# Performance work log

Measured on AMD Instinct MI355X. Metric: run time of the kernel, lower is better.

The kernel has to match this reference:

```python
import jax, jax.numpy as jnp
import numpy as np

N_NODES = 50000
N_EDGES = 800000
EDGE_F = 96
NODE_F = 256
GLOB_F = 64
HIDDEN = 1024
N_GRAPHS = 8
MLP_IN = NODE_F + 3 * EDGE_F + GLOB_F  # 608


def setup_inputs() -> dict:
    key = jax.random.key(0)
    ks = jax.random.split(key, 9)
    x = jax.random.normal(ks[0], (N_NODES, NODE_F), dtype=jnp.float32)
    edge_attr = jax.random.normal(ks[1], (N_EDGES, EDGE_F), dtype=jnp.float32)
    u = jax.random.normal(ks[2], (N_GRAPHS, GLOB_F), dtype=jnp.float32)
    W1 = jax.random.normal(ks[3], (MLP_IN, HIDDEN), dtype=jnp.float32) * (1.0 / np.sqrt(MLP_IN))
    b1 = jax.random.normal(ks[4], (HIDDEN,), dtype=jnp.float32) * 0.01
    W2 = jax.random.normal(ks[5], (HIDDEN, NODE_F), dtype=jnp.float32) * (1.0 / np.sqrt(HIDDEN))
    b2 = jax.random.normal(ks[6], (NODE_F,), dtype=jnp.float32) * 0.01
    edge_index = jax.random.randint(ks[7], (2, N_EDGES), 0, N_NODES, dtype=jnp.int64 if jax.config.jax_enable_x64 else jnp.int32)
    batch = jnp.sort(jax.random.randint(ks[8], (N_NODES,), 0, N_GRAPHS, dtype=jnp.int32))
    return {"x": x, "edge_attr": edge_attr, "u": u, "W1": W1, "b1": b1,
            "W2": W2, "b2": b2, "edge_index": edge_index, "batch": batch}


def reference(x, edge_attr, u, W1, b1, W2, b2, edge_index, batch):
    col = edge_index[1]  # destination node for each edge
    n = x.shape[0]
    # sum / max / mean segment reductions over edges -> per-node features
    out1 = jax.ops.segment_sum(edge_attr, col, num_segments=n)                     # [N, E_F]
    cnt = jax.ops.segment_sum(jnp.ones((edge_attr.shape[0], 1), edge_attr.dtype), col, num_segments=n)  # [N,1]
    out2 = jax.ops.segment_max(edge_attr, col, num_segments=n)
    out2 = jnp.where(cnt > 0, out2, jnp.zeros_like(out2))  # torch_scatter gives 0 for empty segments
    out3 = out1 / jnp.maximum(cnt, 1.0)                    # mean; 0 for empty segments
    h = jnp.concatenate([x, out1, out2, out3, u[batch]], axis=1)  # [N, 608]
    h = jax.nn.relu(h @ W1 + b1) @ W2 + b2                        # node MLP
    return h + x  # residual
```

## Files before the change

### kernel.cpp

```cpp
#include <hip/hip_runtime.h>
#include <stdint.h>

#define N_NODES 50000
#define N_EDGES 800000
#define EDGE_F  96
#define NODE_F  256
#define GLOB_F  64
#define HIDDEN  1024
#define MLP_IN  608
#define M_PAD   50048

typedef __bf16 bf16;
typedef __bf16 bf16x8 __attribute__((ext_vector_type(8)));
typedef float  f32x4  __attribute__((ext_vector_type(4)));

typedef __attribute__((address_space(1))) unsigned int gu32;
typedef __attribute__((address_space(3))) unsigned int lu32;

__device__ __forceinline__ void glds16(const void* g, void* l) {
    __builtin_amdgcn_global_load_lds((const gu32*)g, (lu32*)l, 16, 0, 0);
}

static constexpr size_t H_OFF    = 0;
static constexpr size_t H_BYTES  = (size_t)M_PAD * MLP_IN * 2;
static constexpr size_t HID_OFF  = H_OFF + H_BYTES;
static constexpr size_t HID_BYTES= (size_t)M_PAD * HIDDEN * 2;
static constexpr size_t W1T_OFF  = HID_OFF + HID_BYTES;
static constexpr size_t W1T_BYTES= (size_t)HIDDEN * MLP_IN * 2;
static constexpr size_t W2T_OFF  = W1T_OFF + W1T_BYTES;
static constexpr size_t W2T_BYTES= (size_t)NODE_F * HIDDEN * 2;
static constexpr size_t DEG_OFF  = W2T_OFF + W2T_BYTES;
static constexpr size_t DEG_BYTES= 200192;
static constexpr size_t CUR_OFF  = DEG_OFF + DEG_BYTES;
static constexpr size_t CUR_BYTES= 200192;
static constexpr size_t START_OFF= CUR_OFF + CUR_BYTES;
static constexpr size_t START_BYTES = 200192;
static constexpr size_t EIDS_OFF = START_OFF + START_BYTES;
static constexpr size_t EIDS_BYTES = (size_t)N_EDGES * 4;

__global__ __launch_bounds__(256) void hist_kernel(const int* __restrict__ col,
                                                   int* __restrict__ deg) {
    int e = blockIdx.x * 256 + threadIdx.x;
    if (e < N_EDGES) atomicAdd(&deg[col[e]], 1);
}

__global__ __launch_bounds__(1024) void scan_kernel(const int* __restrict__ deg,
                                                    int* __restrict__ start) {
    __shared__ int partial[1024];
    const int t = threadIdx.x;
    const int CH = 49;
    int base = t * CH;
    int s = 0;
    for (int i = 0; i < CH; i++) {
        int idx = base + i;
        if (idx < N_NODES) s += deg[idx];
    }
    partial[t] = s;
    __syncthreads();
    for (int off = 1; off < 1024; off <<= 1) {
        int v = (t >= off) ? partial[t - off] : 0;
        __syncthreads();
        partial[t] += v;
        __syncthreads();
    }
    int run = (t == 0) ? 0 : partial[t - 1];
    for (int i = 0; i < CH; i++) {
        int idx = base + i;
        if (idx < N_NODES) { start[idx] = run; run += deg[idx]; }
    }
    if (t == 1023) start[N_NODES] = run;
}

__global__ __launch_bounds__(256) void scatter_kernel(const int* __restrict__ col,
                                                      const int* __restrict__ start,
                                                      int* __restrict__ cursor,
                                                      int* __restrict__ eids) {
    int e = blockIdx.x * 256 + threadIdx.x;
    if (e < N_EDGES) {
        int c = col[e];
        int p = start[c] + atomicAdd(&cursor[c], 1);
        eids[p] = e;
    }
}

#define BH_CHUNK 128
__global__ __launch_bounds__(128) void build_h_kernel(const float* __restrict__ x,
                                                      const float* __restrict__ edge_attr,
                                                      const float* __restrict__ u,
                                                      const int* __restrict__ batch,
                                                      const int* __restrict__ start,
                                                      const int* __restrict__ eids,
                                                      bf16* __restrict__ H) {
    const int n = blockIdx.x;
    const int t = threadIdx.x;
    bf16* row = H + (size_t)n * MLP_IN;
    if (n >= N_NODES) {
        for (int c = t; c < MLP_IN; c += 128) row[c] = (bf16)0.0f;
        return;
    }
    if (t < 64) {
        float4 v = ((const float4*)(x + (size_t)n * NODE_F))[t];
        row[t * 4 + 0] = (bf16)v.x;
        row[t * 4 + 1] = (bf16)v.y;
        row[t * 4 + 2] = (bf16)v.z;
        row[t * 4 + 3] = (bf16)v.w;
    } else {
        int g = batch[n];
        row[544 + (t - 64)] = (bf16)u[g * GLOB_F + (t - 64)];
    }

    __shared__ int se[BH_CHUNK];
    const int s0 = start[n], s1 = start[n + 1];
    float sm = 0.0f, mx = -3.0e38f;
    for (int base = s0; base < s1; base += BH_CHUNK) {
        const int cnt = min(BH_CHUNK, s1 - base);
        __syncthreads();
        if (t < cnt) se[t] = eids[base + t];
        __syncthreads();
        if (t < EDGE_F) {
            int i = 0;
            for (; i + 4 <= cnt; i += 4) {
                float v0 = edge_attr[(size_t)se[i + 0] * EDGE_F + t];
                float v1 = edge_attr[(size_t)se[i + 1] * EDGE_F + t];
                float v2 = edge_attr[(size_t)se[i + 2] * EDGE_F + t];
                float v3 = edge_attr[(size_t)se[i + 3] * EDGE_F + t];
                sm += (v0 + v1) + (v2 + v3);
                mx = fmaxf(mx, fmaxf(fmaxf(v0, v1), fmaxf(v2, v3)));
            }
            for (; i < cnt; i++) {
                float v = edge_attr[(size_t)se[i] * EDGE_F + t];
                sm += v;
                mx = fmaxf(mx, v);
            }
        }
    }
    if (t < EDGE_F) {
        int d = s1 - s0;
        if (d == 0) mx = 0.0f;
        float mean = sm / fmaxf((float)d, 1.0f);
        row[256 + t] = (bf16)sm;
        row[352 + t] = (bf16)mx;
        row[448 + t] = (bf16)mean;
    }
}

__global__ __launch_bounds__(256) void convert_w_kernel(const float* __restrict__ W1,
                                                        const float* __restrict__ W2,
                                                        bf16* __restrict__ W1t,
                                                        bf16* __restrict__ W2t) {
    int i = blockIdx.x * 256 + threadIdx.x;
    if (i < HIDDEN * MLP_IN) {
        int n = i / MLP_IN, k = i - n * MLP_IN;
        W1t[i] = (bf16)W1[(size_t)k * HIDDEN + n];
    }
    if (i < NODE_F * HIDDEN) {
        int n = i / HIDDEN, k = i - n * HIDDEN;
        W2t[i] = (bf16)W2[(size_t)k * NODE_F + n];
    }
}

__global__ __launch_bounds__(256) void gemm1_kernel(const bf16* __restrict__ H,
                                                    const bf16* __restrict__ Wt,
                                                    const float* __restrict__ b1,
                                                    bf16* __restrict__ hid) {
    __shared__ __align__(16) bf16 As[128 * 32];
    __shared__ __align__(16) bf16 Bs[128 * 32];
    const int t = threadIdx.x;
    const int wave = t >> 6, lane = t & 63;
    const int quad = lane >> 4, l16 = lane & 15;
    const int wm = (wave & 1) << 6, wn = (wave >> 1) << 6;
    const int bm = blockIdx.x, bn = blockIdx.y;

    f32x4 acc[4][4] = {};

    const char* Ag = (const char*)H  + (size_t)bm * 128 * (MLP_IN * 2);
    const char* Bg = (const char*)Wt + (size_t)bn * 128 * (MLP_IN * 2);
    const int srow = t >> 2, scc = t & 3;
    const size_t rowoff = (size_t)srow * (MLP_IN * 2) + scc * 16;
    char* Al = (char*)As + t * 16;
    char* Bl = (char*)Bs + t * 16;

    for (int k0 = 0; k0 < MLP_IN; k0 += 32) {
        __syncthreads();
        const char* a0 = Ag + rowoff + k0 * 2;
        glds16(a0, Al);
        glds16(a0 + (size_t)64 * (MLP_IN * 2), Al + 4096);
        const char* b0 = Bg + rowoff + k0 * 2;
        glds16(b0, Bl);
        glds16(b0 + (size_t)64 * (MLP_IN * 2), Bl + 4096);
        __syncthreads();
        bf16x8 a[4], b[4];
#pragma unroll
        for (int i = 0; i < 4; i++) a[i] = *(const bf16x8*)&As[(wm + i * 16 + l16) * 32 + quad * 8];
#pragma unroll
        for (int i = 0; i < 4; i++) b[i] = *(const bf16x8*)&Bs[(wn + i * 16 + l16) * 32 + quad * 8];
#pragma unroll
        for (int i = 0; i < 4; i++)
#pragma unroll
            for (int j = 0; j < 4; j++)
                acc[i][j] = __builtin_amdgcn_mfma_f32_16x16x32_bf16(a[i], b[j], acc[i][j], 0, 0, 0);
    }
#pragma unroll
    for (int i = 0; i < 4; i++) {
        int row0 = bm * 128 + wm + i * 16 + quad * 4;
#pragma unroll
        for (int j = 0; j < 4; j++) {
            int col = bn * 128 + wn + j * 16 + l16;
            float bias = b1[col];
#pragma unroll
            for (int r = 0; r < 4; r++) {
                float v = acc[i][j][r] + bias;
                v = fmaxf(v, 0.0f);
                hid[(size_t)(row0 + r) * HIDDEN + col] = (bf16)v;
            }
        }
    }
}

__global__ __launch_bounds__(256) void gemm2_kernel(const bf16* __restrict__ Hd,
                                                    const bf16* __restrict__ Wt,
                                                    const float* __restrict__ b2,
                                                    const float* __restrict__ x,
                                                    float* __restrict__ out) {
    __shared__ __align__(16) bf16 As[128 * 32];
    __shared__ __align__(16) bf16 Bs[128 * 32];
    const int t = threadIdx.x;
    const int wave = t >> 6, lane = t & 63;
    const int quad = lane >> 4, l16 = lane & 15;
    const int wm = (wave & 1) << 6, wn = (wave >> 1) << 6;
    const int bm = blockIdx.x, bn = blockIdx.y;

    f32x4 acc[4][4] = {};

    const char* Ag = (const char*)Hd + (size_t)bm * 128 * (HIDDEN * 2);
    const char* Bg = (const char*)Wt + (size_t)bn * 128 * (HIDDEN * 2);
    const int srow = t >> 2, scc = t & 3;
    const size_t rowoff = (size_t)srow * (HIDDEN * 2) + scc * 16;
    char* Al = (char*)As + t * 16;
    char* Bl = (char*)Bs + t * 16;

    for (int k0 = 0; k0 < HIDDEN; k0 += 32) {
        __syncthreads();
        const char* a0 = Ag + rowoff + k0 * 2;
        glds16(a0, Al);
        glds16(a0 + (size_t)64 * (HIDDEN * 2), Al + 4096);
        const char* b0 = Bg + rowoff + k0 * 2;
        glds16(b0, Bl);
        glds16(b0 + (size_t)64 * (HIDDEN * 2), Bl + 4096);
        __syncthreads();
        bf16x8 a[4], b[4];
#pragma unroll
        for (int i = 0; i < 4; i++) a[i] = *(const bf16x8*)&As[(wm + i * 16 + l16) * 32 + quad * 8];
#pragma unroll
        for (int i = 0; i < 4; i++) b[i] = *(const bf16x8*)&Bs[(wn + i * 16 + l16) * 32 + quad * 8];
#pragma unroll
        for (int i = 0; i < 4; i++)
#pragma unroll
            for (int j = 0; j < 4; j++)
                acc[i][j] = __builtin_amdgcn_mfma_f32_16x16x32_bf16(a[i], b[j], acc[i][j], 0, 0, 0);
    }
#pragma unroll
    for (int i = 0; i < 4; i++) {
        int row0 = bm * 128 + wm + i * 16 + quad * 4;
#pragma unroll
        for (int j = 0; j < 4; j++) {
            int col = bn * 128 + wn + j * 16 + l16;
            float bias = b2[col];
#pragma unroll
            for (int r = 0; r < 4; r++) {
                int row = row0 + r;
                if (row < N_NODES) {
                    size_t idx = (size_t)row * NODE_F + col;
                    out[idx] = acc[i][j][r] + bias + x[idx];
                }
            }
        }
    }
}

extern "C" void kernel_launch(void* const* d_in, const int* in_sizes, int n_in,
                              void* d_out, int out_size, void* d_ws, size_t ws_size,
                              hipStream_t stream) {
    const float* x         = (const float*)d_in[0];
    const float* edge_attr = (const float*)d_in[1];
    const float* u         = (const float*)d_in[2];
    const float* W1        = (const float*)d_in[3];
    const float* b1        = (const float*)d_in[4];
    const float* W2        = (const float*)d_in[5];
    const float* b2        = (const float*)d_in[6];
    const int*   edge_index= (const int*)d_in[7];
    const int*   batch     = (const int*)d_in[8];
    float*       out       = (float*)d_out;

    char* ws = (char*)d_ws;
    bf16* H    = (bf16*)(ws + H_OFF);
    bf16* hid  = (bf16*)(ws + HID_OFF);
    bf16* W1t  = (bf16*)(ws + W1T_OFF);
    bf16* W2t  = (bf16*)(ws + W2T_OFF);
    int*  deg  = (int*)(ws + DEG_OFF);
    int*  cur  = (int*)(ws + CUR_OFF);
    int*  start= (int*)(ws + START_OFF);
    int*  eids = (int*)(ws + EIDS_OFF);

    const int* col = edge_index + N_EDGES;

    hipMemsetAsync(ws + DEG_OFF, 0, DEG_BYTES + CUR_BYTES, stream);
    hist_kernel<<<(N_EDGES + 255) / 256, 256, 0, stream>>>(col, deg);
    scan_kernel<<<1, 1024, 0, stream>>>(deg, start);
    scatter_kernel<<<(N_EDGES + 255) / 256, 256, 0, stream>>>(col, start, cur, eids);
    build_h_kernel<<<M_PAD, 128, 0, stream>>>(x, edge_attr, u, batch, start, eids, H);
    convert_w_kernel<<<(HIDDEN * MLP_IN + 255) / 256, 256, 0, stream>>>(W1, W2, W1t, W2t);
    gemm1_kernel<<<dim3(M_PAD / 128, HIDDEN / 128), 256, 0, stream>>>(H, W1t, b1, hid);
    gemm2_kernel<<<dim3(M_PAD / 128, NODE_F / 128), 256, 0, stream>>>(hid, W2t, b2, x, out);
}
```

Baseline: 879.4 us.

## Parallelize degree scan, tile weight transposes, deepen edge gather unroll

```diff
diff --git a/kernel.cpp b/kernel.cpp
--- a/kernel.cpp
+++ b/kernel.cpp
@@ -9,6 +9,7 @@
 #define HIDDEN  1024
 #define MLP_IN  608
 #define M_PAD   50048
+#define SCAN_BLOCKS 196
 
 typedef __bf16 bf16;
 typedef __bf16 bf16x8 __attribute__((ext_vector_type(8)));
@@ -37,6 +38,9 @@
 static constexpr size_t START_BYTES = 200192;
 static constexpr size_t EIDS_OFF = START_OFF + START_BYTES;
 static constexpr size_t EIDS_BYTES = (size_t)N_EDGES * 4;
+static constexpr size_t BSUM_OFF = EIDS_OFF + EIDS_BYTES;
+static constexpr size_t BSUM_BYTES = 1024;
+static constexpr size_t BOFF_OFF = BSUM_OFF + BSUM_BYTES;
 
 __global__ __launch_bounds__(256) void hist_kernel(const int* __restrict__ col,
                                                    int* __restrict__ deg) {
@@ -44,31 +48,47 @@
     if (e < N_EDGES) atomicAdd(&deg[col[e]], 1);
 }
 
-__global__ __launch_bounds__(1024) void scan_kernel(const int* __restrict__ deg,
-                                                    int* __restrict__ start) {
-    __shared__ int partial[1024];
+__global__ __launch_bounds__(256) void scan_phase1(const int* __restrict__ deg,
+                                                   int* __restrict__ start,
+                                                   int* __restrict__ bsum) {
+    __shared__ int sc[256];
+    const int t = threadIdx.x, b = blockIdx.x;
+    const int idx = b * 256 + t;
+    int v = (idx < N_NODES) ? deg[idx] : 0;
+    sc[t] = v;
+    __syncthreads();
+    for (int off = 1; off < 256; off <<= 1) {
+        int add = (t >= off) ? sc[t - off] : 0;
+        __syncthreads();
+        sc[t] += add;
+        __syncthreads();
+    }
+    if (idx < N_NODES) start[idx] = sc[t] - v;
+    if (t == 255) bsum[b] = sc[255];
+}
+
+__global__ __launch_bounds__(256) void scan_phase2(int* __restrict__ bsum,
+                                                   int* __restrict__ boff,
+                                                   int* __restrict__ start) {
+    __shared__ int sc[256];
     const int t = threadIdx.x;
-    const int CH = 49;
-    int base = t * CH;
-    int s = 0;
-    for (int i = 0; i < CH; i++) {
-        int idx = base + i;
-        if (idx < N_NODES) s += deg[idx];
-    }
-    partial[t] = s;
+    int v = (t < SCAN_BLOCKS) ? bsum[t] : 0;
+    sc[t] = v;
     __syncthreads();
-    for (int off = 1; off < 1024; off <<= 1) {
-        int v = (t >= off) ? partial[t - off] : 0;
-        __syncthreads();
-        partial[t] += v;
-        __syncthreads();
-    }
-    int run = (t == 0) ? 0 : partial[t - 1];
-    for (int i = 0; i < CH; i++) {
-        int idx = base + i;
-        if (idx < N_NODES) { start[idx] = run; run += deg[idx]; }
-    }
-    if (t == 1023) start[N_NODES] = run;
+    for (int off = 1; off < 256; off <<= 1) {
+        int add = (t >= off) ? sc[t - off] : 0;
+        __syncthreads();
+        sc[t] += add;
+        __syncthreads();
+    }
+    if (t < SCAN_BLOCKS) boff[t] = sc[t] - v;
+    if (t == 255) start[N_NODES] = sc[255];
+}
+
+__global__ __launch_bounds__(256) void scan_phase3(int* __restrict__ start,
+                                                   const int* __restrict__ boff) {
+    const int idx = blockIdx.x * 256 + threadIdx.x;
+    if (idx < N_NODES) start[idx] += boff[blockIdx.x];
 }
 
 __global__ __launch_bounds__(256) void scatter_kernel(const int* __restrict__ col,
@@ -119,15 +139,27 @@
         __syncthreads();
         if (t < EDGE_F) {
             int i = 0;
-            for (; i + 4 <= cnt; i += 4) {
+            for (; i + 8 <= cnt; i += 8) {
                 float v0 = edge_attr[(size_t)se[i + 0] * EDGE_F + t];
                 float v1 = edge_attr[(size_t)se[i + 1] * EDGE_F + t];
                 float v2 = edge_attr[(size_t)se[i + 2] * EDGE_F + t];
                 float v3 = edge_attr[(size_t)se[i + 3] * EDGE_F + t];
-                sm += (v0 + v1) + (v2 + v3);
-                mx = fmaxf(mx, fmaxf(fmaxf(v0, v1), fmaxf(v2, v3)));
-            }
-            for (; i < cnt; i++) {
+                float v4 = edge_attr[(size_t)se[i + 4] * EDGE_F + t];
+                float v5 = edge_attr[(size_t)se[i + 5] * EDGE_F + t];
+                float v6 = edge_attr[(size_t)se[i + 6] * EDGE_F + t];
+                float v7 = edge_attr[(size_t)se[i + 7] * EDGE_F + t];
+                sm += ((v0 + v1) + (v2 + v3)) + ((v4 + v5) + (v6 + v7));
+                float m01 = fmaxf(v0, v1), m23 = fmaxf(v2, v3);
+                float m45 = fmaxf(v4, v5), m67 = fmaxf(v6, v7);
+                mx = fmaxf(mx, fmaxf(fmaxf(m01, m23), fmaxf(m45, m67)));
+            }
+            for (; i + 2 <= cnt; i += 2) {
+                float v0 = edge_attr[(size_t)se[i + 0] * EDGE_F + t];
+                float v1 = edge_attr[(size_t)se[i + 1] * EDGE_F + t];
+                sm += v0 + v1;
+                mx = fmaxf(mx, fmaxf(v0, v1));
+            }
+            if (i < cnt) {
                 float v = edge_attr[(size_t)se[i] * EDGE_F + t];
                 sm += v;
                 mx = fmaxf(mx, v);
@@ -144,19 +176,19 @@
     }
 }
 
-__global__ __launch_bounds__(256) void convert_w_kernel(const float* __restrict__ W1,
-                                                        const float* __restrict__ W2,
-                                                        bf16* __restrict__ W1t,
-                                                        bf16* __restrict__ W2t) {
-    int i = blockIdx.x * 256 + threadIdx.x;
-    if (i < HIDDEN * MLP_IN) {
-        int n = i / MLP_IN, k = i - n * MLP_IN;
-        W1t[i] = (bf16)W1[(size_t)k * HIDDEN + n];
-    }
-    if (i < NODE_F * HIDDEN) {
-        int n = i / HIDDEN, k = i - n * HIDDEN;
-        W2t[i] = (bf16)W2[(size_t)k * NODE_F + n];
-    }
+__global__ __launch_bounds__(256) void transpose_kernel(const float* __restrict__ W,
+                                                        bf16* __restrict__ Wt,
+                                                        int K, int N) {
+    __shared__ float tile[32][33];
+    const int tx = threadIdx.x & 31, ty = threadIdx.x >> 5;
+    const int n0 = blockIdx.x * 32, k0 = blockIdx.y * 32;
+#pragma unroll
+    for (int r = 0; r < 4; r++)
+        tile[ty + 8 * r][tx] = W[(size_t)(k0 + ty + 8 * r) * N + (n0 + tx)];
+    __syncthreads();
+#pragma unroll
+    for (int r = 0; r < 4; r++)
+        Wt[(size_t)(n0 + ty + 8 * r) * K + (k0 + tx)] = (bf16)tile[tx][ty + 8 * r];
 }
 
 __global__ __launch_bounds__(256) void gemm1_kernel(const bf16* __restrict__ H,
@@ -301,15 +333,20 @@
     int*  cur  = (int*)(ws + CUR_OFF);
     int*  start= (int*)(ws + START_OFF);
     int*  eids = (int*)(ws + EIDS_OFF);
+    int*  bsum = (int*)(ws + BSUM_OFF);
+    int*  boff = (int*)(ws + BOFF_OFF);
 
     const int* col = edge_index + N_EDGES;
 
     hipMemsetAsync(ws + DEG_OFF, 0, DEG_BYTES + CUR_BYTES, stream);
     hist_kernel<<<(N_EDGES + 255) / 256, 256, 0, stream>>>(col, deg);
-    scan_kernel<<<1, 1024, 0, stream>>>(deg, start);
+    scan_phase1<<<SCAN_BLOCKS, 256, 0, stream>>>(deg, start, bsum);
+    scan_phase2<<<1, 256, 0, stream>>>(bsum, boff, start);
+    scan_phase3<<<SCAN_BLOCKS, 256, 0, stream>>>(start, boff);
     scatter_kernel<<<(N_EDGES + 255) / 256, 256, 0, stream>>>(col, start, cur, eids);
     build_h_kernel<<<M_PAD, 128, 0, stream>>>(x, edge_attr, u, batch, start, eids, H);
-    convert_w_kernel<<<(HIDDEN * MLP_IN + 255) / 256, 256, 0, stream>>>(W1, W2, W1t, W2t);
+    transpose_kernel<<<dim3(HIDDEN / 32, MLP_IN / 32), 256, 0, stream>>>(W1, W1t, MLP_IN, HIDDEN);
+    transpose_kernel<<<dim3(NODE_F / 32, HIDDEN / 32), 256, 0, stream>>>(W2, W2t, HIDDEN, NODE_F);
     gemm1_kernel<<<dim3(M_PAD / 128, HIDDEN / 128), 256, 0, stream>>>(H, W1t, b1, hid);
     gemm2_kernel<<<dim3(M_PAD / 128, NODE_F / 128), 256, 0, stream>>>(hid, W2t, b2, x, out);
 }
```

Result: faster. 792.6 us (-9.9%).
